# Optimization experiments

Measured on AMD Instinct MI355X. Metric: run time of the kernel, lower is better.

Reference implementation:

```python
import jax, jax.numpy as jnp
import numpy as np

NUM_HEADS = 12
HEAD_DIM = 64
SCALE = HEAD_DIM ** -0.5


def setup_inputs() -> dict:
    key = jax.random.key(0)
    k1, k2, k3, k4, k5 = jax.random.split(key, 5)
    B, N, C = 4, 2048, NUM_HEADS * HEAD_DIM
    x = jax.random.normal(k1, (B, N, C), dtype=jnp.float32)
    W_qkv = jax.random.normal(k2, (C, 3 * C), dtype=jnp.float32) * (C ** -0.5)
    b_qkv = jax.random.normal(k3, (3 * C,), dtype=jnp.float32) * 0.02
    W_proj = jax.random.normal(k4, (C, C), dtype=jnp.float32) * (C ** -0.5)
    b_proj = jax.random.normal(k5, (C,), dtype=jnp.float32) * 0.02
    return {"x": x, "W_qkv": W_qkv, "b_qkv": b_qkv, "W_proj": W_proj, "b_proj": b_proj}


def reference(x, W_qkv, b_qkv, W_proj, b_proj):
    B, N, C = x.shape
    H, D = NUM_HEADS, HEAD_DIM
    qkv = x @ W_qkv + b_qkv                      # [B, N, 3C]
    qkv = qkv.reshape(B, N, 3, H, D)
    q = qkv[:, :, 0].transpose(0, 2, 1, 3) * SCALE  # [B, H, N, D]
    k = qkv[:, :, 1].transpose(0, 2, 1, 3)          # [B, H, N, D]
    v = qkv[:, :, 2].transpose(0, 2, 1, 3)          # [B, H, N, D]
    attn = jnp.einsum("bhnd,bhmd->bhnm", q, k)   # [B, H, N, N]
    attn = jax.nn.softmax(attn, axis=-1)
    ctx = jnp.einsum("bhnm,bhmd->bhnd", attn, v)  # [B, H, N, D]
    attn_out = ctx.transpose(0, 2, 1, 3).reshape(B, N, C)
    out = attn_out @ W_proj + b_proj
    return (out, attn_out)
```

## Files before the change

kernel.cpp:

```cpp
#include <hip/hip_runtime.h>
#include <stdint.h>

typedef unsigned short u16;
using bf16x8 = __attribute__((ext_vector_type(8))) __bf16;
using s16x8  = __attribute__((ext_vector_type(8))) short;
using f32x4  = __attribute__((ext_vector_type(4))) float;

#define SCALE_Q 0.125f
#define LOG2E 1.44269504088896f

__device__ __forceinline__ u16 f2bf(float f) {
  union { float f; uint32_t u; } v; v.f = f;
  uint32_t u = v.u;
  return (u16)((u + 0x7FFFu + ((u >> 16) & 1)) >> 16);
}

__device__ __forceinline__ bf16x8 ld_frag(const u16* p) {
  return __builtin_bit_cast(bf16x8, *(const s16x8*)p);
}

__device__ __forceinline__ f32x4 MF(bf16x8 a, bf16x8 b, f32x4 c) {
  return __builtin_amdgcn_mfma_f32_16x16x32_bf16(a, b, c, 0, 0, 0);
}

__device__ __forceinline__ void gld16(const u16* g, u16* l) {
  __builtin_amdgcn_global_load_lds(
      (const __attribute__((address_space(1))) uint32_t*)g,
      (__attribute__((address_space(3))) uint32_t*)l, 16, 0, 0);
}

__device__ __forceinline__ uint32_t pk_bf16(float a, float b) {
  uint32_t u0 = __builtin_bit_cast(uint32_t, a) + 0x8000u;
  uint32_t u1 = __builtin_bit_cast(uint32_t, b) + 0x8000u;
  return __builtin_amdgcn_perm(u1, u0, 0x07060302u);
}

__global__ void prep_kernel(const float* __restrict__ x, u16* __restrict__ xb,
                            const float* __restrict__ Wq, u16* __restrict__ wqt,
                            const float* __restrict__ Wp, u16* __restrict__ wpt) {
  __shared__ float tile[32][33];
  int bx = blockIdx.x;
  if (bx < 6144) {
    int i = (bx * 256 + threadIdx.x) * 4;
    float4 v = *(const float4*)(x + i);
    uint2 o;
    o.x = (uint32_t)f2bf(v.x) | ((uint32_t)f2bf(v.y) << 16);
    o.y = (uint32_t)f2bf(v.z) | ((uint32_t)f2bf(v.w) << 16);
    *(uint2*)(xb + i) = o;
    return;
  }
  bx -= 6144;
  const float* in;
  u16* out;
  int C, cb, rb;
  const int R = 768;
  if (bx < 1728) { in = Wq; out = wqt; C = 2304; cb = bx % 72; rb = bx / 72; }
  else { bx -= 1728; in = Wp; out = wpt; C = 768; cb = bx % 24; rb = bx / 24; }
  int c0 = cb * 32, r0 = rb * 32;
  int tx = threadIdx.x & 31, ty = threadIdx.x >> 5;
#pragma unroll
  for (int j = 0; j < 32; j += 8)
    tile[ty + j][tx] = in[(size_t)(r0 + ty + j) * C + c0 + tx];
  __syncthreads();
#pragma unroll
  for (int j = 0; j < 32; j += 8)
    out[(size_t)(c0 + ty + j) * R + r0 + tx] = f2bf(tile[tx][ty + j]);
}

__global__ __launch_bounds__(256) void gemm_qkv(
    const u16* __restrict__ A, const u16* __restrict__ Bt, const float* __restrict__ bias,
    u16* __restrict__ q_out, u16* __restrict__ k_out, u16* __restrict__ v_out) {
  constexpr int K = 768;
  __shared__ __align__(16) u16 smem[17408];
  u16* sA = smem;
  u16* sB = smem + 8192;
  const int tid = threadIdx.x;
  const int lane = tid & 63, wave = tid >> 6;
  const int ml = lane & 15, kg = lane >> 4;
  const int wr = wave >> 1, wc = wave & 1;
  const int bn = blockIdx.x, bm = blockIdx.y;

  f32x4 acc[4][4] = {};
  const u16* Abase = A + (size_t)(bm * 128) * K;
  const u16* Bbase = Bt + (size_t)(bn * 128) * K;

  for (int k0 = 0; k0 < K; k0 += 64) {
#pragma unroll
    for (int p = 0; p < 4; p++) {
      int q = p * 256 + tid;
      int r = q >> 3, s = q & 7, c = s ^ (r & 7);
      gld16(Abase + (size_t)r * K + k0 + c * 8, sA + q * 8);
      gld16(Bbase + (size_t)r * K + k0 + c * 8, sB + q * 8);
    }
    __syncthreads();
#pragma unroll
    for (int kc = 0; kc < 2; kc++) {
      bf16x8 af[4], bfr[4];
      int ac = kc * 4 + kg;
#pragma unroll
      for (int i = 0; i < 4; i++) {
        int arow = wr * 64 + i * 16 + ml;
        af[i] = ld_frag(sA + (arow * 8 + (ac ^ (arow & 7))) * 8);
        int brow = wc * 64 + i * 16 + ml;
        bfr[i] = ld_frag(sB + (brow * 8 + (ac ^ (brow & 7))) * 8);
      }
#pragma unroll
      for (int mi = 0; mi < 4; mi++)
#pragma unroll
        for (int ni = 0; ni < 4; ni++)
          acc[mi][ni] = MF(af[mi], bfr[ni], acc[mi][ni]);
    }
    __syncthreads();
  }

  if (bn >= 12) {
    uint32_t* t32 = (uint32_t*)smem;
#pragma unroll
    for (int ni = 0; ni < 4; ni++) {
      int n_local = wc * 64 + ni * 16 + ml;
      float bv = bias[bn * 128 + n_local];
#pragma unroll
      for (int mi = 0; mi < 4; mi++) {
        int mh = wr * 32 + mi * 8 + kg * 2;
        t32[n_local * 68 + mh]     = pk_bf16(acc[mi][ni][0] + bv, acc[mi][ni][1] + bv);
        t32[n_local * 68 + mh + 1] = pk_bf16(acc[mi][ni][2] + bv, acc[mi][ni][3] + bv);
      }
    }
    __syncthreads();
    int row = tid >> 1, seg = tid & 1;
    int dg = (bn - 12) * 128 + row;
    int h = dg >> 6, d = dg & 63;
    int bi = bm >> 4, tok0 = (bm & 15) * 128;
    u16* dst = v_out + ((size_t)(bi * 12 + h) * 64 + d) * 2048 + tok0 + seg * 64;
    const uint32_t* src = t32 + row * 68 + seg * 32;
#pragma unroll
    for (int j = 0; j < 8; j++)
      *(uint4*)(dst + j * 8) = *(const uint4*)(src + j * 4);
  } else {
    u16* dst = (bn < 6) ? q_out : k_out;
    float scl = (bn < 6) ? SCALE_Q * LOG2E : 1.0f;
#pragma unroll
    for (int ni = 0; ni < 4; ni++) {
      int n = bn * 128 + wc * 64 + ni * 16 + ml;
      int rem = (bn < 6) ? n : n - 768;
      int h = rem >> 6, d = rem & 63;
      float bv = bias[n];
#pragma unroll
      for (int mi = 0; mi < 4; mi++) {
        int m0 = bm * 128 + wr * 64 + mi * 16 + kg * 4;
#pragma unroll
        for (int r = 0; r < 4; r++) {
          int m = m0 + r;
          int bi = m >> 11, tok = m & 2047;
          dst[(size_t)(bi * 12 + h) * 131072 + (size_t)tok * 64 + d] = f2bf((acc[mi][ni][r] + bv) * scl);
        }
      }
    }
  }
}

__global__ __launch_bounds__(256) void gemm_proj(
    const u16* __restrict__ A, const u16* __restrict__ Bt, const float* __restrict__ bias,
    float* __restrict__ c_out) {
  constexpr int K = 768;
  __shared__ __align__(16) u16 sA[128 * 64];
  __shared__ __align__(16) u16 sB[64 * 64];
  const int tid = threadIdx.x;
  const int lane = tid & 63, wave = tid >> 6;
  const int ml = lane & 15, kg = lane >> 4;
  const int bn = blockIdx.x, bm = blockIdx.y;
  f32x4 acc[2][4] = {};
  const u16* Abase = A + (size_t)(bm * 128) * K;
  const u16* Bbase = Bt + (size_t)(bn * 64) * K;

  for (int k0 = 0; k0 < K; k0 += 64) {
#pragma unroll
    for (int p = 0; p < 4; p++) {
      int q = p * 256 + tid;
      int r = q >> 3, s = q & 7, c = s ^ (r & 7);
      gld16(Abase + (size_t)r * K + k0 + c * 8, sA + q * 8);
    }
#pragma unroll
    for (int p = 0; p < 2; p++) {
      int q = p * 256 + tid;
      int r = q >> 3, s = q & 7, c = s ^ (r & 7);
      gld16(Bbase + (size_t)r * K + k0 + c * 8, sB + q * 8);
    }
    __syncthreads();
#pragma unroll
    for (int kc = 0; kc < 2; kc++) {
      int ac = kc * 4 + kg;
      bf16x8 af[2], bfr[4];
#pragma unroll
      for (int i = 0; i < 2; i++) {
        int arow = wave * 32 + i * 16 + ml;
        af[i] = ld_frag(sA + (arow * 8 + (ac ^ (arow & 7))) * 8);
      }
#pragma unroll
      for (int i = 0; i < 4; i++) {
        int brow = i * 16 + ml;
        bfr[i] = ld_frag(sB + (brow * 8 + (ac ^ (brow & 7))) * 8);
      }
#pragma unroll
      for (int mi = 0; mi < 2; mi++)
#pragma unroll
        for (int ni = 0; ni < 4; ni++)
          acc[mi][ni] = MF(af[mi], bfr[ni], acc[mi][ni]);
    }
    __syncthreads();
  }
#pragma unroll
  for (int ni = 0; ni < 4; ni++) {
    int n = bn * 64 + ni * 16 + ml;
    float bv = bias[n];
#pragma unroll
    for (int mi = 0; mi < 2; mi++) {
      int m0 = bm * 128 + wave * 32 + mi * 16 + kg * 4;
#pragma unroll
      for (int r = 0; r < 4; r++)
        c_out[(size_t)(m0 + r) * 768 + n] = acc[mi][ni][r] + bv;
    }
  }
}

__global__ __launch_bounds__(256, 3) void attn_kernel(
    const u16* __restrict__ qs, const u16* __restrict__ ks, const u16* __restrict__ vt,
    float* __restrict__ attn_f32, u16* __restrict__ attn_bf) {
  __shared__ __align__(16) u16 sK[2][4096];
  __shared__ __align__(16) u16 sV[2][4096];
  __shared__ __align__(16) u16 sP[4][2304];
  const int tid = threadIdx.x, lane = tid & 63, wave = tid >> 6;
  const int ml = lane & 15, kg = lane >> 4;
  const int bh = blockIdx.y;
  const int q0 = blockIdx.x * 128 + wave * 32;
  const size_t base = (size_t)bh * 131072;

  bf16x8 qf[2][2];
#pragma unroll
  for (int qt = 0; qt < 2; qt++) {
    const u16* qp = qs + base + (size_t)(q0 + qt * 16 + ml) * 64 + kg * 8;
    qf[qt][0] = ld_frag(qp);
    qf[qt][1] = ld_frag(qp + 32);
  }
  f32x4 l4[2] = {};
  f32x4 O[2][4] = {};

  const int m7 = ml & 7;
  const u16* kbase[2] = { &sK[0][ml * 64 + ((0 + kg) ^ m7) * 8],
                          &sK[0][ml * 64 + ((4 + kg) ^ m7) * 8] };
  const u16* vbase[2] = { &sV[0][ml * 64 + ((0 + kg) ^ m7) * 8],
                          &sV[0][ml * 64 + ((4 + kg) ^ m7) * 8] };
  u16* pw = &sP[wave][ml * 72 + kg * 4];
  const u16* pr = &sP[wave][ml * 72 + kg * 8];

  const int r0 = tid >> 3,          c0 = (tid & 7) ^ (r0 & 7);
  const int r1 = (256 + tid) >> 3,  c1 = (tid & 7) ^ (r1 & 7);
  const u16* kgp0 = ks + base + r0 * 64 + c0 * 8;
  const u16* kgp1 = ks + base + r1 * 64 + c1 * 8;
  const u16* vgp0 = vt + base + r0 * 2048 + c0 * 8;
  const u16* vgp1 = vt + base + r1 * 2048 + c1 * 8;

  auto stage = [&](int b, int kt) {
    gld16(kgp0 + kt * 64, &sK[b][tid * 8]);
    gld16(kgp1 + kt * 64, &sK[b][2048 + tid * 8]);
    gld16(vgp0 + kt,      &sV[b][tid * 8]);
    gld16(vgp1 + kt,      &sV[b][2048 + tid * 8]);
  };

  stage(0, 0);
  for (int kt = 0; kt < 2048; kt += 128) {
#pragma unroll
    for (int half = 0; half < 2; half++) {
      const int cur = kt + half * 64;
      __syncthreads();
      if (cur + 64 < 2048) stage(half ^ 1, cur + 64);

      f32x4 sc[2][4] = {};
#pragma unroll
      for (int nt = 0; nt < 4; nt++)
#pragma unroll
        for (int kc = 0; kc < 2; kc++) {
          bf16x8 kf = ld_frag(kbase[kc] + nt * 1024 + half * 4096);
          sc[0][nt] = MF(kf, qf[0][kc], sc[0][nt]);
          sc[1][nt] = MF(kf, qf[1][kc], sc[1][nt]);
        }

#pragma unroll
      for (int qt = 0; qt < 2; qt++)
#pragma unroll
        for (int nt = 0; nt < 4; nt++) {
          f32x4 p;
#pragma unroll
          for (int r = 0; r < 4; r++) p[r] = __builtin_amdgcn_exp2f(sc[qt][nt][r]);
          l4[qt] += p;
          uint2 w;
          w.x = pk_bf16(p[0], p[1]);
          w.y = pk_bf16(p[2], p[3]);
          *(uint2*)(pw + qt * 1152 + nt * 16) = w;
        }

      asm volatile("s_waitcnt lgkmcnt(0)" ::: "memory");

#pragma unroll
      for (int kc = 0; kc < 2; kc++) {
        bf16x8 pf0 = ld_frag(pr + kc * 32);
        bf16x8 pf1 = ld_frag(pr + 1152 + kc * 32);
#pragma unroll
        for (int nt2 = 0; nt2 < 4; nt2++) {
          bf16x8 vf = ld_frag(vbase[kc] + nt2 * 1024 + half * 4096);
          O[0][nt2] = MF(pf0, vf, O[0][nt2]);
          O[1][nt2] = MF(pf1, vf, O[1][nt2]);
        }
      }
    }
  }

  float linv[2];
#pragma unroll
  for (int qt = 0; qt < 2; qt++) {
    float s = l4[qt][0] + l4[qt][1] + l4[qt][2] + l4[qt][3];
    s += __shfl_xor(s, 16);
    s += __shfl_xor(s, 32);
    linv[qt] = __builtin_amdgcn_rcpf(s);
  }
  int b = bh / 12, h = bh - b * 12;
#pragma unroll
  for (int qt = 0; qt < 2; qt++)
#pragma unroll
    for (int r = 0; r < 4; r++) {
      float inv = __shfl(linv[qt], kg * 4 + r, 64);
      int qrow = q0 + qt * 16 + kg * 4 + r;
      size_t rowoff = ((size_t)(b * 2048 + qrow)) * 768 + h * 64;
#pragma unroll
      for (int nt2 = 0; nt2 < 4; nt2++) {
        float v = O[qt][nt2][r] * inv;
        int d = nt2 * 16 + ml;
        attn_f32[rowoff + d] = v;
        attn_bf[rowoff + d] = f2bf(v);
      }
    }
}

extern "C" void kernel_launch(void* const* d_in, const int* in_sizes, int n_in,
                              void* d_out, int out_size, void* d_ws, size_t ws_size,
                              hipStream_t stream) {
  const float* x      = (const float*)d_in[0];
  const float* W_qkv  = (const float*)d_in[1];
  const float* b_qkv  = (const float*)d_in[2];
  const float* W_proj = (const float*)d_in[3];
  const float* b_proj = (const float*)d_in[4];
  float* out      = (float*)d_out;
  float* attn_out = out + (size_t)8192 * 768;

  char* ws = (char*)d_ws;
  const size_t SZ_XB = (size_t)8192 * 768 * 2;
  u16* xb      = (u16*)(ws);
  u16* wqkv_t  = (u16*)(ws + SZ_XB);
  u16* wproj_t = (u16*)(ws + SZ_XB + 3538944);
  u16* qs      = (u16*)(ws + SZ_XB + 3538944 + 1179648);
  u16* ks      = (u16*)((char*)qs + SZ_XB);
  u16* vt      = (u16*)((char*)ks + SZ_XB);
  u16* ab      = xb;

  prep_kernel<<<6144 + 1728 + 576, 256, 0, stream>>>(x, xb, W_qkv, wqkv_t, W_proj, wproj_t);
  gemm_qkv<<<dim3(18, 64), 256, 0, stream>>>(xb, wqkv_t, b_qkv, qs, ks, vt);
  attn_kernel<<<dim3(16, 48), 256, 0, stream>>>(qs, ks, vt, attn_out, ab);
  gemm_proj<<<dim3(12, 64), 256, 0, stream>>>(ab, wproj_t, b_proj, out);
}
```

Measured before the change: 228.1 us.

## Use 32x32 MFMA in attention, pass P via lane shuffles, remap blocks to XCDs

Rewrites the attention inner loop to use 32x32x16 bf16 MFMAs computing transposed scores (K as A operand), so each lane owns one query row. The P matrix is converted into the B operand for the PV MFMA through a cross-half lane shuffle instead of a round trip through shared memory, which removes the sP buffer and an lgkmcnt wait. Block IDs are remapped so that blocks sharing a batch-head land on the same XCD for L2 reuse, and the output stores become vectorised float4 and uint2 writes. The new operand layout and swizzle must match exactly, and the final bf16 store now rounds with pk_bf16 instead of f2bf.

New measurement: 235.5 us. 1.03x slower.

```diff
diff --git a/kernel.cpp b/kernel.cpp
--- a/kernel.cpp
+++ b/kernel.cpp
@@ -5,6 +5,7 @@
 using bf16x8 = __attribute__((ext_vector_type(8))) __bf16;
 using s16x8  = __attribute__((ext_vector_type(8))) short;
 using f32x4  = __attribute__((ext_vector_type(4))) float;
+using f32x16 = __attribute__((ext_vector_type(16))) float;
 
 #define SCALE_Q 0.125f
 #define LOG2E 1.44269504088896f
@@ -21,6 +22,9 @@
 
 __device__ __forceinline__ f32x4 MF(bf16x8 a, bf16x8 b, f32x4 c) {
   return __builtin_amdgcn_mfma_f32_16x16x32_bf16(a, b, c, 0, 0, 0);
+}
+__device__ __forceinline__ f32x16 MF32(bf16x8 a, bf16x8 b, f32x16 c) {
+  return __builtin_amdgcn_mfma_f32_32x32x16_bf16(a, b, c, 0, 0, 0);
 }
 
 __device__ __forceinline__ void gld16(const u16* g, u16* l) {
@@ -228,33 +232,30 @@
     float* __restrict__ attn_f32, u16* __restrict__ attn_bf) {
   __shared__ __align__(16) u16 sK[2][4096];
   __shared__ __align__(16) u16 sV[2][4096];
-  __shared__ __align__(16) u16 sP[4][2304];
   const int tid = threadIdx.x, lane = tid & 63, wave = tid >> 6;
-  const int ml = lane & 15, kg = lane >> 4;
-  const int bh = blockIdx.y;
-  const int q0 = blockIdx.x * 128 + wave * 32;
+  const int c31 = lane & 31, h = lane >> 5;
+
+  int id = blockIdx.y * 16 + blockIdx.x;
+  int xcd = id & 7, slot = id >> 3;
+  int bh = xcd * 6 + (slot >> 4);
+  int qb = slot & 15;
+  const int q0w = qb * 128 + wave * 32;
   const size_t base = (size_t)bh * 131072;
 
-  bf16x8 qf[2][2];
-#pragma unroll
-  for (int qt = 0; qt < 2; qt++) {
-    const u16* qp = qs + base + (size_t)(q0 + qt * 16 + ml) * 64 + kg * 8;
-    qf[qt][0] = ld_frag(qp);
-    qf[qt][1] = ld_frag(qp + 32);
-  }
-  f32x4 l4[2] = {};
-  f32x4 O[2][4] = {};
-
-  const int m7 = ml & 7;
-  const u16* kbase[2] = { &sK[0][ml * 64 + ((0 + kg) ^ m7) * 8],
-                          &sK[0][ml * 64 + ((4 + kg) ^ m7) * 8] };
-  const u16* vbase[2] = { &sV[0][ml * 64 + ((0 + kg) ^ m7) * 8],
-                          &sV[0][ml * 64 + ((4 + kg) ^ m7) * 8] };
-  u16* pw = &sP[wave][ml * 72 + kg * 4];
-  const u16* pr = &sP[wave][ml * 72 + kg * 8];
-
-  const int r0 = tid >> 3,          c0 = (tid & 7) ^ (r0 & 7);
-  const int r1 = (256 + tid) >> 3,  c1 = (tid & 7) ^ (r1 & 7);
+  bf16x8 qf[4];
+#pragma unroll
+  for (int kc = 0; kc < 4; kc++)
+    qf[kc] = ld_frag(qs + base + (size_t)(q0w + c31) * 64 + kc * 16 + h * 8);
+
+  f32x4 lacc = {};
+  f32x16 O0 = {}, O1 = {};
+
+  const int kx8 = ((h ^ (c31 & 7))) * 8;
+  const u16* kR = &sK[0][c31 * 64];
+  const u16* vR = &sV[0][c31 * 64];
+
+  const int r0 = tid >> 3,         c0 = (tid & 7) ^ (r0 & 7);
+  const int r1 = (256 + tid) >> 3, c1 = (tid & 7) ^ (r1 & 7);
   const u16* kgp0 = ks + base + r0 * 64 + c0 * 8;
   const u16* kgp1 = ks + base + r1 * 64 + c1 * 8;
   const u16* vgp0 = vt + base + r0 * 2048 + c0 * 8;
@@ -275,70 +276,71 @@
       __syncthreads();
       if (cur + 64 < 2048) stage(half ^ 1, cur + 64);
 
-      f32x4 sc[2][4] = {};
-#pragma unroll
-      for (int nt = 0; nt < 4; nt++)
-#pragma unroll
-        for (int kc = 0; kc < 2; kc++) {
-          bf16x8 kf = ld_frag(kbase[kc] + nt * 1024 + half * 4096);
-          sc[0][nt] = MF(kf, qf[0][kc], sc[0][nt]);
-          sc[1][nt] = MF(kf, qf[1][kc], sc[1][nt]);
+      f32x16 S0 = {}, S1 = {};
+#pragma unroll
+      for (int kc = 0; kc < 4; kc++) {
+        const u16* kp = kR + half * 4096 + (kx8 ^ (kc * 16));
+        S0 = MF32(ld_frag(kp),        qf[kc], S0);
+        S1 = MF32(ld_frag(kp + 2048), qf[kc], S1);
+      }
+
+      uint32_t w[2][8], x[2][8];
+#pragma unroll
+      for (int nt = 0; nt < 2; nt++) {
+        const f32x16& S = nt ? S1 : S0;
+#pragma unroll
+        for (int g = 0; g < 4; g++) {
+          float p0 = __builtin_amdgcn_exp2f(S[4 * g + 0]);
+          float p1 = __builtin_amdgcn_exp2f(S[4 * g + 1]);
+          float p2 = __builtin_amdgcn_exp2f(S[4 * g + 2]);
+          float p3 = __builtin_amdgcn_exp2f(S[4 * g + 3]);
+          lacc[0] += p0; lacc[1] += p1; lacc[2] += p2; lacc[3] += p3;
+          w[nt][2 * g]     = pk_bf16(p0, p1);
+          w[nt][2 * g + 1] = pk_bf16(p2, p3);
         }
-
-#pragma unroll
-      for (int qt = 0; qt < 2; qt++)
-#pragma unroll
-        for (int nt = 0; nt < 4; nt++) {
-          f32x4 p;
-#pragma unroll
-          for (int r = 0; r < 4; r++) p[r] = __builtin_amdgcn_exp2f(sc[qt][nt][r]);
-          l4[qt] += p;
-          uint2 w;
-          w.x = pk_bf16(p[0], p[1]);
-          w.y = pk_bf16(p[2], p[3]);
-          *(uint2*)(pw + qt * 1152 + nt * 16) = w;
-        }
-
-      asm volatile("s_waitcnt lgkmcnt(0)" ::: "memory");
-
-#pragma unroll
-      for (int kc = 0; kc < 2; kc++) {
-        bf16x8 pf0 = ld_frag(pr + kc * 32);
-        bf16x8 pf1 = ld_frag(pr + 1152 + kc * 32);
-#pragma unroll
-        for (int nt2 = 0; nt2 < 4; nt2++) {
-          bf16x8 vf = ld_frag(vbase[kc] + nt2 * 1024 + half * 4096);
-          O[0][nt2] = MF(pf0, vf, O[0][nt2]);
-          O[1][nt2] = MF(pf1, vf, O[1][nt2]);
-        }
-      }
-    }
-  }
-
-  float linv[2];
-#pragma unroll
-  for (int qt = 0; qt < 2; qt++) {
-    float s = l4[qt][0] + l4[qt][1] + l4[qt][2] + l4[qt][3];
-    s += __shfl_xor(s, 16);
-    s += __shfl_xor(s, 32);
-    linv[qt] = __builtin_amdgcn_rcpf(s);
-  }
-  int b = bh / 12, h = bh - b * 12;
-#pragma unroll
-  for (int qt = 0; qt < 2; qt++)
-#pragma unroll
-    for (int r = 0; r < 4; r++) {
-      float inv = __shfl(linv[qt], kg * 4 + r, 64);
-      int qrow = q0 + qt * 16 + kg * 4 + r;
-      size_t rowoff = ((size_t)(b * 2048 + qrow)) * 768 + h * 64;
-#pragma unroll
-      for (int nt2 = 0; nt2 < 4; nt2++) {
-        float v = O[qt][nt2][r] * inv;
-        int d = nt2 * 16 + ml;
-        attn_f32[rowoff + d] = v;
-        attn_bf[rowoff + d] = f2bf(v);
-      }
-    }
+      }
+#pragma unroll
+      for (int nt = 0; nt < 2; nt++)
+#pragma unroll
+        for (int i = 0; i < 8; i++)
+          x[nt][i] = (uint32_t)__shfl_xor((int)w[nt][i], 32);
+
+#pragma unroll
+      for (int ksi = 0; ksi < 4; ksi++) {
+        int nt = ksi >> 1, s4 = (ksi & 1) * 4;
+        uint32_t b0 = h ? x[nt][s4 + 2] : w[nt][s4 + 0];
+        uint32_t b1 = h ? x[nt][s4 + 3] : w[nt][s4 + 1];
+        uint32_t b2 = h ? w[nt][s4 + 2] : x[nt][s4 + 0];
+        uint32_t b3 = h ? w[nt][s4 + 3] : x[nt][s4 + 1];
+        uint4 ub = {b0, b1, b2, b3};
+        bf16x8 pf = __builtin_bit_cast(bf16x8, ub);
+        const u16* vp = vR + half * 4096 + (kx8 ^ (ksi * 16));
+        O0 = MF32(ld_frag(vp),        pf, O0);
+        O1 = MF32(ld_frag(vp + 2048), pf, O1);
+      }
+    }
+  }
+
+  float l = lacc[0] + lacc[1] + lacc[2] + lacc[3];
+  l += __shfl_xor(l, 32);
+  float inv = __builtin_amdgcn_rcpf(l);
+  int b = bh / 12, hh = bh - b * 12;
+  size_t rowoff = ((size_t)(b * 2048 + q0w + c31)) * 768 + hh * 64;
+#pragma unroll
+  for (int dt = 0; dt < 2; dt++) {
+    const f32x16& Ot = dt ? O1 : O0;
+#pragma unroll
+    for (int g = 0; g < 4; g++) {
+      int d0 = dt * 32 + g * 8 + h * 4;
+      float4 o4 = {Ot[4 * g + 0] * inv, Ot[4 * g + 1] * inv,
+                   Ot[4 * g + 2] * inv, Ot[4 * g + 3] * inv};
+      *(float4*)(attn_f32 + rowoff + d0) = o4;
+      uint2 wv;
+      wv.x = pk_bf16(o4.x, o4.y);
+      wv.y = pk_bf16(o4.z, o4.w);
+      *(uint2*)(attn_bf + rowoff + d0) = wv;
+    }
+  }
 }
 
 extern "C" void kernel_launch(void* const* d_in, const int* in_sizes, int n_in,
```
